# Performance work log

Measured on AMD Instinct MI355X. Metric: run time of the kernel, lower is better.

## Reference

```python
import jax, jax.numpy as jnp
import numpy as np
import math

HEADS = 8
CH = 16  # hidden_channels per head
SCALE = 1.0 / math.sqrt(CH)


def _transformer_conv(x, src, dst, qw, qb, kw, kb, vw, vb, sw, sb):
    """PyG TransformerConv (concat=True, root_weight=True, eval mode -> no dropout)."""
    N = x.shape[0]
    q = (x @ qw + qb).reshape(N, HEADS, CH)
    k = (x @ kw + kb).reshape(N, HEADS, CH)
    v = (x @ vw + vb).reshape(N, HEADS, CH)
    # per-edge attention logits: message from src j to dst i
    alpha = jnp.sum(q[dst] * k[src], axis=-1) * SCALE        # [E, H]
    # segment softmax over incoming edges of each dst node
    m = jax.ops.segment_max(alpha, dst, num_segments=N)      # [N, H]
    a = jnp.exp(alpha - m[dst])                              # [E, H]
    denom = jax.ops.segment_sum(a, dst, num_segments=N)      # [N, H]
    a = a / denom[dst]
    msg = v[src] * a[:, :, None]                             # [E, H, C]
    out = jax.ops.segment_sum(msg, dst, num_segments=N).reshape(N, HEADS * CH)
    return out + x @ sw + sb  # skip connection (lin_skip)


def setup_inputs() -> dict:
    key = jax.random.key(0)
    ks = jax.random.split(key, 16)
    N, E, IN = 50000, 800000, 128
    D = HEADS * CH  # 128

    def lin(k, fi, fo):
        return (jax.random.normal(k, (fi, fo), jnp.float32) / math.sqrt(fi))

    inp = {
        "x": jax.random.normal(ks[0], (N, IN), jnp.float32),
        "edge_index": jax.random.randint(ks[1], (2, E), 0, N, dtype=jnp.int64),
        "edge_attr": jax.random.normal(ks[2], (E, 1), jnp.float32),
        # conv1: in_channels -> hidden*heads
        "q_w0": lin(ks[3], IN, D), "q_b0": jnp.zeros((D,), jnp.float32),
        "k_w0": lin(ks[4], IN, D), "k_b0": jnp.zeros((D,), jnp.float32),
        "v_w0": lin(ks[5], IN, D), "v_b0": jnp.zeros((D,), jnp.float32),
        "s_w0": lin(ks[6], IN, D), "s_b0": jnp.zeros((D,), jnp.float32),
        # conv2[0]: hidden*heads -> hidden*heads
        "q_w1": lin(ks[7], D, D), "q_b1": jnp.zeros((D,), jnp.float32),
        "k_w1": lin(ks[8], D, D), "k_b1": jnp.zeros((D,), jnp.float32),
        "v_w1": lin(ks[9], D, D), "v_b1": jnp.zeros((D,), jnp.float32),
        "s_w1": lin(ks[10], D, D), "s_b1": jnp.zeros((D,), jnp.float32),
    }
    return inp


def reference(x, edge_index, edge_attr,
              q_w0, q_b0, k_w0, k_b0, v_w0, v_b0, s_w0, s_b0,
              q_w1, q_b1, k_w1, k_b1, v_w1, v_b1, s_w1, s_b1):
    src, dst = edge_index[0], edge_index[1]
    # edge_attr is accepted but unused by the original forward
    h = _transformer_conv(x, src, dst, q_w0, q_b0, k_w0, k_b0, v_w0, v_b0, s_w0, s_b0)
    h = jax.nn.relu(h)
    h = _transformer_conv(h, src, dst, q_w1, q_b1, k_w1, k_b1, v_w1, v_b1, s_w1, s_b1)
    return h
```

## Files before the change

### kernel.cpp

```cpp
#include <hip/hip_runtime.h>
#include <math.h>


#define HEADS 8
#define CH 16
#define DM 128
#define SCALE 0.25f

typedef __attribute__((ext_vector_type(8))) short short8;
typedef __attribute__((ext_vector_type(4))) float floatx4;
typedef __attribute__((ext_vector_type(2))) float floatx2;

static __device__ __forceinline__ ushort f2bf(float f) {
    unsigned u = __float_as_uint(f);
    unsigned r = u + 0x7FFFu + ((u >> 16) & 1u);
    return (ushort)(r >> 16);
}
static __device__ __forceinline__ float bflo(unsigned u) {
    return __uint_as_float(u << 16);
}
static __device__ __forceinline__ float bfhi(unsigned u) {
    return __uint_as_float(u & 0xFFFF0000u);
}
static __device__ __forceinline__ unsigned pack2bf(float lo, float hi) {
    return (unsigned)f2bf(lo) | ((unsigned)f2bf(hi) << 16);
}
static __device__ __forceinline__ floatx2 fp8lo(unsigned v) {
    return __builtin_amdgcn_cvt_pk_f32_fp8(v, false);
}
static __device__ __forceinline__ floatx2 fp8hi(unsigned v) {
    return __builtin_amdgcn_cvt_pk_f32_fp8(v, true);
}

#define AP 136

static __device__ __forceinline__ void gemm_body(
    int bx, const float* __restrict__ Xf, const ushort* __restrict__ Xb,
    const ushort* __restrict__ WT,
    const float* __restrict__ bq, const float* __restrict__ bk,
    const float* __restrict__ bv, const float* __restrict__ bsk,
    ushort* __restrict__ Qb, ushort* __restrict__ Kb,
    unsigned char* __restrict__ Vq, ushort* __restrict__ Sb, int N,
    ushort* As)
{
    const int row0 = bx * 32;
    const int tid  = threadIdx.x;

    if (Xf) {
        #pragma unroll
        for (int i = 0; i < 2; ++i) {
            int id = tid + i * 512;
            int r = id >> 5, ch = id & 31;
            float4 v = make_float4(0.f, 0.f, 0.f, 0.f);
            if (row0 + r < N)
                v = *(const float4*)(Xf + (size_t)(row0 + r) * DM + ch * 4);
            ushort4 sv;
            sv.x = f2bf(v.x); sv.y = f2bf(v.y);
            sv.z = f2bf(v.z); sv.w = f2bf(v.w);
            *(ushort4*)(As + r * AP + ch * 4) = sv;
        }
    } else {
        int id = tid;
        int r = id >> 4, ch = id & 15;
        uint4 v = make_uint4(0, 0, 0, 0);
        if (row0 + r < N)
            v = *(const uint4*)(Xb + (size_t)(row0 + r) * DM + ch * 8);
        *(uint4*)(As + r * AP + ch * 8) = v;
    }
    __syncthreads();

    const int lane = tid & 63, w = tid >> 6;
    const int band = w & 3;
    const int m0   = (w >> 2) * 2;
    const int lr = lane & 15, lq = lane >> 4;

    short8 a[4][2];
    #pragma unroll
    for (int ks = 0; ks < 4; ++ks) {
        const int koff = ks * 32 + lq * 8;
        #pragma unroll
        for (int mt = 0; mt < 2; ++mt)
            a[ks][mt] = *(const short8*)(As + (mt * 16 + lr) * AP + koff);
    }

    #pragma unroll
    for (int mi = 0; mi < 2; ++mi) {
        const int mat = m0 + mi;
        const ushort* Wband = WT + (size_t)mat * 16384 + (size_t)band * 4096;
        const float* bias = (mat == 0) ? bq : (mat == 1) ? bk
                          : (mat == 2) ? bv : bsk;
        floatx4 acc[2][2] = {};
        #pragma unroll
        for (int ks = 0; ks < 4; ++ks) {
            short8 b[2];
            #pragma unroll
            for (int t = 0; t < 2; ++t)
                b[t] = *(const short8*)(Wband + (ks * 2 + t) * 512 + lane * 8);
            #pragma unroll
            for (int mt = 0; mt < 2; ++mt)
                #pragma unroll
                for (int nt = 0; nt < 2; ++nt)
                    acc[mt][nt] = __builtin_amdgcn_mfma_f32_16x16x32_bf16(
                        a[ks][mt], b[nt], acc[mt][nt], 0, 0, 0);
        }
        const int nq = band * 32;
        if (mat == 2) {
            #pragma unroll
            for (int nt = 0; nt < 2; ++nt) {
                const int col = nq + nt * 16 + lr;
                const float bcol = bias[col];
                #pragma unroll
                for (int mt = 0; mt < 2; ++mt) {
                    const int rbase0 = row0 + mt * 16 + lq * 4;
                    #pragma unroll
                    for (int r = 0; r < 4; ++r) {
                        const int row = rbase0 + r;
                        if (row < N) {
                            float v = acc[mt][nt][r] + bcol;
                            unsigned p = __builtin_amdgcn_cvt_pk_fp8_f32(
                                v, v, 0u, false);
                            Vq[(size_t)row * DM + col] = (unsigned char)p;
                        }
                    }
                }
            }
        } else {
            ushort* OutB = (mat == 0) ? Qb : (mat == 1) ? Kb : Sb;
            #pragma unroll
            for (int nt = 0; nt < 2; ++nt) {
                const int col = nq + nt * 16 + lr;
                const float bcol = bias[col];
                #pragma unroll
                for (int mt = 0; mt < 2; ++mt) {
                    const int rbase0 = row0 + mt * 16 + lq * 4;
                    #pragma unroll
                    for (int r = 0; r < 4; ++r) {
                        const int row = rbase0 + r;
                        if (row < N)
                            OutB[(size_t)row * DM + col] = f2bf(acc[mt][nt][r] + bcol);
                    }
                }
            }
        }
    }
}

__global__ __launch_bounds__(256)
void cvt_hist(const float* __restrict__ W0, const float* __restrict__ W1,
              const float* __restrict__ W2, const float* __restrict__ W3,
              const float* __restrict__ W4, const float* __restrict__ W5,
              const float* __restrict__ W6, const float* __restrict__ W7,
              ushort* __restrict__ WT,
              const int* __restrict__ dst, int* __restrict__ counts, int E)
{
    const int b = blockIdx.x;
    if (b < 512) {
        const float* Ws[8] = {W0, W1, W2, W3, W4, W5, W6, W7};
        const float* W = Ws[b >> 6];
        int idx = (b & 63) * 256 + threadIdx.x;
        int c    = idx >> 9;
        int s    = idx & 511;
        int lane = s >> 3, j = s & 7;
        int w  = c >> 3, ks = (c >> 1) & 3, t = c & 1;
        int n = w * 32 + t * 16 + (lane & 15);
        int k = ks * 32 + (lane >> 4) * 8 + j;
        WT[(size_t)(b >> 6) * 16384 + idx] = f2bf(W[k * 128 + n]);
    } else {
        int e4 = ((b - 512) * 256 + threadIdx.x) * 4;
        if (e4 + 3 < E) {
            const int4 d = *(const int4*)(dst + e4);
            atomicAdd(&counts[d.x], 1);
            atomicAdd(&counts[d.y], 1);
            atomicAdd(&counts[d.z], 1);
            atomicAdd(&counts[d.w], 1);
        } else {
            for (int e = e4; e < E; ++e) atomicAdd(&counts[dst[e]], 1);
        }
    }
}

__global__ __launch_bounds__(256)
void scan_p1(const int* __restrict__ counts, int* __restrict__ rowptr,
             int* __restrict__ bsums, int* __restrict__ dbins, int N)
{
    __shared__ int s[256];
    __shared__ int lb[256];
    const int t = threadIdx.x;
    const int base = blockIdx.x * 1024 + t * 4;
    lb[t] = 0;
    int c[4];
    int sum = 0;
    #pragma unroll
    for (int j = 0; j < 4; ++j) {
        c[j] = (base + j < N) ? counts[base + j] : 0;
        sum += c[j];
    }
    s[t] = sum;
    __syncthreads();
    #pragma unroll
    for (int j = 0; j < 4; ++j)
        if (base + j < N) atomicAdd(&lb[min(c[j], 255)], 1);
    for (int off = 1; off < 256; off <<= 1) {
        int v = (t >= off) ? s[t - off] : 0;
        __syncthreads();
        if (t >= off) s[t] += v;
        __syncthreads();
    }
    int ex = (t == 0) ? 0 : s[t - 1];
    #pragma unroll
    for (int j = 0; j < 4; ++j) {
        if (base + j < N) rowptr[base + j] = ex;
        ex += c[j];
    }
    if (t == 255) bsums[blockIdx.x] = s[255];
    if (lb[t] > 0) atomicAdd(&dbins[t], lb[t]);
}

__global__ __launch_bounds__(256)
void scan_p2(const int* __restrict__ bsums, int* __restrict__ bbase, int nb,
             const int* __restrict__ dbins, int* __restrict__ dcur)
{
    __shared__ int s[256];
    const int t = threadIdx.x;
    s[t] = (t < nb) ? bsums[t] : 0;
    __syncthreads();
    for (int off = 1; off < 256; off <<= 1) {
        int v = (t >= off) ? s[t - off] : 0;
        __syncthreads();
        if (t >= off) s[t] += v;
        __syncthreads();
    }
    if (t <= nb) bbase[t] = (t == 0) ? 0 : s[t - 1];
    __syncthreads();
    s[t] = dbins[255 - t];
    __syncthreads();
    for (int off = 1; off < 256; off <<= 1) {
        int v = (t >= off) ? s[t - off] : 0;
        __syncthreads();
        if (t >= off) s[t] += v;
        __syncthreads();
    }
    dcur[255 - t] = (t == 0) ? 0 : s[t - 1];
}

__global__ __launch_bounds__(256)
void scan_p3(int* __restrict__ rowptr, int* __restrict__ cursor,
             const int* __restrict__ bbase, int* __restrict__ bcur,
             int N, int nb)
{
    int i = blockIdx.x * 256 + threadIdx.x;
    if (i < N) {
        int v = rowptr[i] + bbase[i >> 10];
        rowptr[i] = v;
        cursor[i] = v;
        if ((i & 255) == 0) bcur[i >> 8] = v;
    }
    if (i == 0) rowptr[N] = bbase[nb];
}

__global__ __launch_bounds__(512)
void gemm_scat(const float* __restrict__ Xf, const ushort* __restrict__ Xb,
               const ushort* __restrict__ WT,
               const float* __restrict__ bq, const float* __restrict__ bk,
               const float* __restrict__ bv, const float* __restrict__ bsk,
               ushort* __restrict__ Qb, ushort* __restrict__ Kb,
               unsigned char* __restrict__ Vq, ushort* __restrict__ Sb, int N,
               const int* __restrict__ src, const int* __restrict__ dst,
               int* __restrict__ cursor, int* __restrict__ esrc,
               int* __restrict__ ebuf, int* __restrict__ bcur,
               const int* __restrict__ counts, int* __restrict__ dcur,
               int* __restrict__ perm, int E, int sb, int db, int bucketed)
{
    __shared__ ushort As[32 * AP];
    __shared__ int lc[256];
    __shared__ int lbase[256];

    const int b = blockIdx.x;
    if (b < sb) {
        if (bucketed) {
            const int t = threadIdx.x;
            if (t < 256) lc[t] = 0;
            __syncthreads();
            int e4 = (b * 512 + t) * 4;
            int pk[4], bkt[4];
            int ne = 0;
            if (e4 + 3 < E) {
                const int4 s = *(const int4*)(src + e4);
                const int4 d = *(const int4*)(dst + e4);
                pk[0] = (s.x & 0xFFFF) | ((d.x & 255) << 16); bkt[0] = d.x >> 8;
                pk[1] = (s.y & 0xFFFF) | ((d.y & 255) << 16); bkt[1] = d.y >> 8;
                pk[2] = (s.z & 0xFFFF) | ((d.z & 255) << 16); bkt[2] = d.z >> 8;
                pk[3] = (s.w & 0xFFFF) | ((d.w & 255) << 16); bkt[3] = d.w >> 8;
                ne = 4;
            } else {
                for (int e = e4; e < E; ++e) {
                    int sv = src[e], dv = dst[e];
                    pk[ne] = (sv & 0xFFFF) | ((dv & 255) << 16);
                    bkt[ne] = dv >> 8;
                    ++ne;
                }
            }
            for (int j = 0; j < ne; ++j) atomicAdd(&lc[bkt[j]], 1);
            __syncthreads();
            if (t < 256 && lc[t] > 0) lbase[t] = atomicAdd(&bcur[t], lc[t]);
            __syncthreads();
            if (t < 256) lc[t] = 0;
            __syncthreads();
            for (int j = 0; j < ne; ++j) {
                int r = atomicAdd(&lc[bkt[j]], 1);
                ebuf[lbase[bkt[j]] + r] = pk[j];
            }
        } else {
            int e4 = (b * 512 + (int)threadIdx.x) * 4;
            if (e4 + 3 < E) {
                const int4 s = *(const int4*)(src + e4);
                const int4 d = *(const int4*)(dst + e4);
                esrc[atomicAdd(&cursor[d.x], 1)] = s.x;
                esrc[atomicAdd(&cursor[d.y], 1)] = s.y;
                esrc[atomicAdd(&cursor[d.z], 1)] = s.z;
                esrc[atomicAdd(&cursor[d.w], 1)] = s.w;
            } else {
                for (int e = e4; e < E; ++e) {
                    int pos = atomicAdd(&cursor[dst[e]], 1);
                    esrc[pos] = src[e];
                }
            }
        }
    } else if (b < sb + db) {
        const int t = threadIdx.x;
        if (t < 256) lc[t] = 0;
        __syncthreads();
        const int n = (b - sb) * 512 + t;
        int bin = 0, rank = 0;
        const bool valid = (n < N);
        if (valid) {
            bin = min(counts[n], 255);
            rank = atomicAdd(&lc[bin], 1);
        }
        __syncthreads();
        if (t < 256 && lc[t] > 0) lbase[t] = atomicAdd(&dcur[t], lc[t]);
        __syncthreads();
        if (valid) perm[lbase[bin] + rank] = n;
    } else {
        gemm_body(b - sb - db, Xf, Xb, WT, bq, bk, bv, bsk,
                  Qb, Kb, Vq, Sb, N, As);
    }
}

__global__ __launch_bounds__(256)
void escat2(const int* __restrict__ rowptr, const int* __restrict__ ebuf,
            int* __restrict__ esrc, int N)
{
    __shared__ int rbase[257];
    __shared__ int cur[256];
    const int b = blockIdx.x, t = threadIdx.x;
    const int n0 = b * 256;
    const int nn = min(256, N - n0);
    rbase[t] = rowptr[min(n0 + t, N)];
    cur[t] = 0;
    if (t == 0) rbase[256] = rowptr[min(n0 + 256, N)];
    __syncthreads();
    const int r0 = rbase[0], r1 = rbase[nn];
    for (int i = r0 + t; i < r1; i += 256) {
        const int e = ebuf[i];
        const int dr = e >> 16;
        const int rank = atomicAdd(&cur[dr], 1);
        esrc[rbase[dr] + rank] = e & 0xFFFF;
    }
}

__global__ __launch_bounds__(512)
void gemm_mfma(const float* __restrict__ Xf, const ushort* __restrict__ Xb,
               const ushort* __restrict__ WT,
               const float* __restrict__ bq, const float* __restrict__ bk,
               const float* __restrict__ bv, const float* __restrict__ bsk,
               ushort* __restrict__ Qb, ushort* __restrict__ Kb,
               unsigned char* __restrict__ Vq, ushort* __restrict__ Sb, int N)
{
    __shared__ ushort As[32 * AP];
    gemm_body(blockIdx.x, Xf, Xb, WT, bq, bk, bv, bsk, Qb, Kb, Vq, Sb, N, As);
}

__global__ __launch_bounds__(256)
void node_attn(const ushort* __restrict__ Qb, const ushort* __restrict__ Kb,
               const unsigned char* __restrict__ Vq,
               const int* __restrict__ rowptr, const int* __restrict__ esrc,
               const int* __restrict__ perm,
               const ushort* __restrict__ Yb, float* __restrict__ Yout,
               ushort* __restrict__ Bout, int N, int relu)
{
    const int idx = blockIdx.x * 8 + (threadIdx.x >> 5);
    if (idx >= N) return;
    const int nid = perm[idx];
    const int c4 = (threadIdx.x & 31) * 4;
    const uint2 qv = *(const uint2*)(Qb + (size_t)nid * DM + c4);
    const float qx = bflo(qv.x), qy = bfhi(qv.x);
    const float qz = bflo(qv.y), qw = bfhi(qv.y);
    const int beg = rowptr[nid], end = rowptr[nid + 1];

    float lA = 0.f, lB = 0.f;
    float a0 = 0.f, a1 = 0.f, a2 = 0.f, a3 = 0.f;
    float b0 = 0.f, b1 = 0.f, b2 = 0.f, b3 = 0.f;

    int i = beg;
    for (; i + 7 < end; i += 8) {
        const int s0 = __builtin_nontemporal_load(esrc + i);
        const int s1 = __builtin_nontemporal_load(esrc + i + 1);
        const int s2 = __builtin_nontemporal_load(esrc + i + 2);
        const int s3 = __builtin_nontemporal_load(esrc + i + 3);
        const int s4 = __builtin_nontemporal_load(esrc + i + 4);
        const int s5 = __builtin_nontemporal_load(esrc + i + 5);
        const int s6 = __builtin_nontemporal_load(esrc + i + 6);
        const int s7 = __builtin_nontemporal_load(esrc + i + 7);
        const uint2 kA = *(const uint2*)(Kb + (size_t)s0 * DM + c4);
        const uint2 kB = *(const uint2*)(Kb + (size_t)s1 * DM + c4);
        const uint2 kC = *(const uint2*)(Kb + (size_t)s2 * DM + c4);
        const uint2 kD = *(const uint2*)(Kb + (size_t)s3 * DM + c4);
        const uint2 kE = *(const uint2*)(Kb + (size_t)s4 * DM + c4);
        const uint2 kF = *(const uint2*)(Kb + (size_t)s5 * DM + c4);
        const uint2 kG = *(const uint2*)(Kb + (size_t)s6 * DM + c4);
        const uint2 kH = *(const uint2*)(Kb + (size_t)s7 * DM + c4);
        const unsigned vA = *(const unsigned*)(Vq + (size_t)s0 * DM + c4);
        const unsigned vB = *(const unsigned*)(Vq + (size_t)s1 * DM + c4);
        const unsigned vC = *(const unsigned*)(Vq + (size_t)s2 * DM + c4);
        const unsigned vD = *(const unsigned*)(Vq + (size_t)s3 * DM + c4);
        const unsigned vE = *(const unsigned*)(Vq + (size_t)s4 * DM + c4);
        const unsigned vF = *(const unsigned*)(Vq + (size_t)s5 * DM + c4);
        const unsigned vG = *(const unsigned*)(Vq + (size_t)s6 * DM + c4);
        const unsigned vH = *(const unsigned*)(Vq + (size_t)s7 * DM + c4);
        float pA = qx * bflo(kA.x);
        pA = fmaf(qy, bfhi(kA.x), pA);
        pA = fmaf(qz, bflo(kA.y), pA);
        pA = fmaf(qw, bfhi(kA.y), pA);
        float pB = qx * bflo(kB.x);
        pB = fmaf(qy, bfhi(kB.x), pB);
        pB = fmaf(qz, bflo(kB.y), pB);
        pB = fmaf(qw, bfhi(kB.y), pB);
        float pC = qx * bflo(kC.x);
        pC = fmaf(qy, bfhi(kC.x), pC);
        pC = fmaf(qz, bflo(kC.y), pC);
        pC = fmaf(qw, bfhi(kC.y), pC);
        float pD = qx * bflo(kD.x);
        pD = fmaf(qy, bfhi(kD.x), pD);
        pD = fmaf(qz, bflo(kD.y), pD);
        pD = fmaf(qw, bfhi(kD.y), pD);
        float pE = qx * bflo(kE.x);
        pE = fmaf(qy, bfhi(kE.x), pE);
        pE = fmaf(qz, bflo(kE.y), pE);
        pE = fmaf(qw, bfhi(kE.y), pE);
        float pF = qx * bflo(kF.x);
        pF = fmaf(qy, bfhi(kF.x), pF);
        pF = fmaf(qz, bflo(kF.y), pF);
        pF = fmaf(qw, bfhi(kF.y), pF);
        float pG = qx * bflo(kG.x);
        pG = fmaf(qy, bfhi(kG.x), pG);
        pG = fmaf(qz, bflo(kG.y), pG);
        pG = fmaf(qw, bfhi(kG.y), pG);
        float pH = qx * bflo(kH.x);
        pH = fmaf(qy, bfhi(kH.x), pH);
        pH = fmaf(qz, bflo(kH.y), pH);
        pH = fmaf(qw, bfhi(kH.y), pH);
        pA += __shfl_xor(pA, 1, 4); pA += __shfl_xor(pA, 2, 4);
        pB += __shfl_xor(pB, 1, 4); pB += __shfl_xor(pB, 2, 4);
        pC += __shfl_xor(pC, 1, 4); pC += __shfl_xor(pC, 2, 4);
        pD += __shfl_xor(pD, 1, 4); pD += __shfl_xor(pD, 2, 4);
        pE += __shfl_xor(pE, 1, 4); pE += __shfl_xor(pE, 2, 4);
        pF += __shfl_xor(pF, 1, 4); pF += __shfl_xor(pF, 2, 4);
        pG += __shfl_xor(pG, 1, 4); pG += __shfl_xor(pG, 2, 4);
        pH += __shfl_xor(pH, 1, 4); pH += __shfl_xor(pH, 2, 4);
        const float wA = __expf(pA * SCALE);
        const float wB = __expf(pB * SCALE);
        const float wC = __expf(pC * SCALE);
        const float wD = __expf(pD * SCALE);
        const float wE = __expf(pE * SCALE);
        const float wF = __expf(pF * SCALE);
        const float wG = __expf(pG * SCALE);
        const float wH = __expf(pH * SCALE);
        lA += (wA + wC) + (wE + wG);
        lB += (wB + wD) + (wF + wH);
        {
            const floatx2 dA0 = fp8lo(vA), dA1 = fp8hi(vA);
            const floatx2 dB0 = fp8lo(vB), dB1 = fp8hi(vB);
            a0 = fmaf(wA, dA0.x, a0); b0 = fmaf(wB, dB0.x, b0);
            a1 = fmaf(wA, dA0.y, a1); b1 = fmaf(wB, dB0.y, b1);
            a2 = fmaf(wA, dA1.x, a2); b2 = fmaf(wB, dB1.x, b2);
            a3 = fmaf(wA, dA1.y, a3); b3 = fmaf(wB, dB1.y, b3);
        }
        {
            const floatx2 dC0 = fp8lo(vC), dC1 = fp8hi(vC);
            const floatx2 dD0 = fp8lo(vD), dD1 = fp8hi(vD);
            a0 = fmaf(wC, dC0.x, a0); b0 = fmaf(wD, dD0.x, b0);
            a1 = fmaf(wC, dC0.y, a1); b1 = fmaf(wD, dD0.y, b1);
            a2 = fmaf(wC, dC1.x, a2); b2 = fmaf(wD, dD1.x, b2);
            a3 = fmaf(wC, dC1.y, a3); b3 = fmaf(wD, dD1.y, b3);
        }
        {
            const floatx2 dE0 = fp8lo(vE), dE1 = fp8hi(vE);
            const floatx2 dF0 = fp8lo(vF), dF1 = fp8hi(vF);
            a0 = fmaf(wE, dE0.x, a0); b0 = fmaf(wF, dF0.x, b0);
            a1 = fmaf(wE, dE0.y, a1); b1 = fmaf(wF, dF0.y, b1);
            a2 = fmaf(wE, dE1.x, a2); b2 = fmaf(wF, dF1.x, b2);
            a3 = fmaf(wE, dE1.y, a3); b3 = fmaf(wF, dF1.y, b3);
        }
        {
            const floatx2 dG0 = fp8lo(vG), dG1 = fp8hi(vG);
            const floatx2 dH0 = fp8lo(vH), dH1 = fp8hi(vH);
            a0 = fmaf(wG, dG0.x, a0); b0 = fmaf(wH, dH0.x, b0);
            a1 = fmaf(wG, dG0.y, a1); b1 = fmaf(wH, dH0.y, b1);
            a2 = fmaf(wG, dG1.x, a2); b2 = fmaf(wH, dH1.x, b2);
            a3 = fmaf(wG, dG1.y, a3); b3 = fmaf(wH, dH1.y, b3);
        }
    }
    for (; i + 3 < end; i += 4) {
        const int s0 = __builtin_nontemporal_load(esrc + i);
        const int s1 = __builtin_nontemporal_load(esrc + i + 1);
        const int s2 = __builtin_nontemporal_load(esrc + i + 2);
        const int s3 = __builtin_nontemporal_load(esrc + i + 3);
        const uint2 kA = *(const uint2*)(Kb + (size_t)s0 * DM + c4);
        const uint2 kB = *(const uint2*)(Kb + (size_t)s1 * DM + c4);
        const uint2 kC = *(const uint2*)(Kb + (size_t)s2 * DM + c4);
        const uint2 kD = *(const uint2*)(Kb + (size_t)s3 * DM + c4);
        const unsigned vA = *(const unsigned*)(Vq + (size_t)s0 * DM + c4);
        const unsigned vB = *(const unsigned*)(Vq + (size_t)s1 * DM + c4);
        const unsigned vC = *(const unsigned*)(Vq + (size_t)s2 * DM + c4);
        const unsigned vD = *(const unsigned*)(Vq + (size_t)s3 * DM + c4);
        float pA = qx * bflo(kA.x);
        pA = fmaf(qy, bfhi(kA.x), pA);
        pA = fmaf(qz, bflo(kA.y), pA);
        pA = fmaf(qw, bfhi(kA.y), pA);
        float pB = qx * bflo(kB.x);
        pB = fmaf(qy, bfhi(kB.x), pB);
        pB = fmaf(qz, bflo(kB.y), pB);
        pB = fmaf(qw, bfhi(kB.y), pB);
        float pC = qx * bflo(kC.x);
        pC = fmaf(qy, bfhi(kC.x), pC);
        pC = fmaf(qz, bflo(kC.y), pC);
        pC = fmaf(qw, bfhi(kC.y), pC);
        float pD = qx * bflo(kD.x);
        pD = fmaf(qy, bfhi(kD.x), pD);
        pD = fmaf(qz, bflo(kD.y), pD);
        pD = fmaf(qw, bfhi(kD.y), pD);
        pA += __shfl_xor(pA, 1, 4); pA += __shfl_xor(pA, 2, 4);
        pB += __shfl_xor(pB, 1, 4); pB += __shfl_xor(pB, 2, 4);
        pC += __shfl_xor(pC, 1, 4); pC += __shfl_xor(pC, 2, 4);
        pD += __shfl_xor(pD, 1, 4); pD += __shfl_xor(pD, 2, 4);
        const float wA = __expf(pA * SCALE);
        const float wB = __expf(pB * SCALE);
        const float wC = __expf(pC * SCALE);
        const float wD = __expf(pD * SCALE);
        lA += wA + wC;
        lB += wB + wD;
        {
            const floatx2 dA0 = fp8lo(vA), dA1 = fp8hi(vA);
            const floatx2 dB0 = fp8lo(vB), dB1 = fp8hi(vB);
            a0 = fmaf(wA, dA0.x, a0); b0 = fmaf(wB, dB0.x, b0);
            a1 = fmaf(wA, dA0.y, a1); b1 = fmaf(wB, dB0.y, b1);
            a2 = fmaf(wA, dA1.x, a2); b2 = fmaf(wB, dB1.x, b2);
            a3 = fmaf(wA, dA1.y, a3); b3 = fmaf(wB, dB1.y, b3);
        }
        {
            const floatx2 dC0 = fp8lo(vC), dC1 = fp8hi(vC);
            const floatx2 dD0 = fp8lo(vD), dD1 = fp8hi(vD);
            a0 = fmaf(wC, dC0.x, a0); b0 = fmaf(wD, dD0.x, b0);
            a1 = fmaf(wC, dC0.y, a1); b1 = fmaf(wD, dD0.y, b1);
            a2 = fmaf(wC, dC1.x, a2); b2 = fmaf(wD, dD1.x, b2);
            a3 = fmaf(wC, dC1.y, a3); b3 = fmaf(wD, dD1.y, b3);
        }
    }
    for (; i < end; ++i) {
        const int s0 = __builtin_nontemporal_load(esrc + i);
        const uint2 kA = *(const uint2*)(Kb + (size_t)s0 * DM + c4);
        const unsigned vA = *(const unsigned*)(Vq + (size_t)s0 * DM + c4);
        float p = qx * bflo(kA.x);
        p = fmaf(qy, bfhi(kA.x), p);
        p = fmaf(qz, bflo(kA.y), p);
        p = fmaf(qw, bfhi(kA.y), p);
        p += __shfl_xor(p, 1, 4);
        p += __shfl_xor(p, 2, 4);
        const float wg = __expf(p * SCALE);
        lA += wg;
        const floatx2 dA0 = fp8lo(vA), dA1 = fp8hi(vA);
        a0 = fmaf(wg, dA0.x, a0);
        a1 = fmaf(wg, dA0.y, a1);
        a2 = fmaf(wg, dA1.x, a2);
        a3 = fmaf(wg, dA1.y, a3);
    }
    const float l = lA + lB;
    a0 += b0; a1 += b1; a2 += b2; a3 += b3;

    const float inv = (l > 0.f) ? 1.f / l : 0.f;
    const uint2 yb = *(const uint2*)(Yb + (size_t)nid * DM + c4);
    float y0 = fmaf(a0, inv, bflo(yb.x));
    float y1 = fmaf(a1, inv, bfhi(yb.x));
    float y2 = fmaf(a2, inv, bflo(yb.y));
    float y3 = fmaf(a3, inv, bfhi(yb.y));
    if (relu) {
        y0 = fmaxf(y0, 0.f); y1 = fmaxf(y1, 0.f);
        y2 = fmaxf(y2, 0.f); y3 = fmaxf(y3, 0.f);
    }
    if (Yout) {
        float4 o = make_float4(y0, y1, y2, y3);
        *(float4*)(Yout + (size_t)nid * DM + c4) = o;
    }
    if (Bout) {
        uint2 o;
        o.x = pack2bf(y0, y1);
        o.y = pack2bf(y2, y3);
        *(uint2*)(Bout + (size_t)nid * DM + c4) = o;
    }
}

extern "C" void kernel_launch(void* const* d_in, const int* in_sizes, int n_in,
                              void* d_out, int out_size, void* d_ws, size_t ws_size,
                              hipStream_t stream)
{
    const float* x   = (const float*)d_in[0];
    const int* eidx  = (const int*)d_in[1];
    const float* qw0 = (const float*)d_in[3];  const float* qb0 = (const float*)d_in[4];
    const float* kw0 = (const float*)d_in[5];  const float* kb0 = (const float*)d_in[6];
    const float* vw0 = (const float*)d_in[7];  const float* vb0 = (const float*)d_in[8];
    const float* sw0 = (const float*)d_in[9];  const float* sb0 = (const float*)d_in[10];
    const float* qw1 = (const float*)d_in[11]; const float* qb1 = (const float*)d_in[12];
    const float* kw1 = (const float*)d_in[13]; const float* kb1 = (const float*)d_in[14];
    const float* vw1 = (const float*)d_in[15]; const float* vb1 = (const float*)d_in[16];
    const float* sw1 = (const float*)d_in[17]; const float* sb1 = (const float*)d_in[18];

    const int N = in_sizes[0] / DM;
    const int E = in_sizes[1] / 2;
    const int* src = eidx;
    const int* dst = eidx + E;

    size_t nd  = (size_t)N * DM;
    ushort* Qb = (ushort*)d_ws;
    ushort* Kb = Qb + nd;
    ushort* Xb = Kb + nd;
    ushort* Sb = Xb + nd;
    ushort* WT = Sb + nd;
    unsigned char* Vq = (unsigned char*)(WT + 8 * 16384);
    int* counts = (int*)(Vq + nd);
    int* rowptr = counts + N;
    int* cursor = rowptr + (N + 1);
    int* esrc   = cursor + N;
    int* perm   = esrc + E;
    int* dbins  = perm + N;
    int* dcur   = dbins + 256;
    int* bsums  = dcur + 256;
    int* bbase  = bsums + 256;
    int* ebuf   = bbase + 257;
    int* bcur   = ebuf + E;
    float* out  = (float*)d_out;

    const int nbuck = (N + 255) >> 8;
    const bool bucketed =
        (N <= 65536) && (nbuck <= 256) &&
        ((uintptr_t)(bcur + 256) <= (uintptr_t)d_ws + ws_size);

    const int nb = (N + 1023) / 1024;
    const int ggrid = (N + 31) / 32;
    const int ablk = (N + 7) / 8;
    const int sb = (E + 2047) / 2048;
    const int db = (N + 511) / 512;

    hipMemsetAsync(counts, 0, (size_t)N * sizeof(int), stream);
    hipMemsetAsync(dbins, 0, 256 * sizeof(int), stream);

    cvt_hist<<<512 + (E + 1023) / 1024, 256, 0, stream>>>(
        qw0, kw0, vw0, sw0, qw1, kw1, vw1, sw1, WT, dst, counts, E);

    scan_p1<<<nb, 256, 0, stream>>>(counts, rowptr, bsums, dbins, N);
    scan_p2<<<1, 256, 0, stream>>>(bsums, bbase, nb, dbins, dcur);
    scan_p3<<<(N + 255) / 256, 256, 0, stream>>>(rowptr, cursor, bbase, bcur,
                                                 N, nb);

    gemm_scat<<<sb + db + ggrid, 512, 0, stream>>>(
        x, nullptr, WT, qb0, kb0, vb0, sb0, Qb, Kb, Vq, Sb, N,
        src, dst, cursor, esrc, ebuf, bcur, counts, dcur, perm,
        E, sb, db, bucketed ? 1 : 0);

    if (bucketed)
        escat2<<<nbuck, 256, 0, stream>>>(rowptr, ebuf, esrc, N);

    node_attn<<<ablk, 256, 0, stream>>>(Qb, Kb, Vq, rowptr, esrc, perm,
                                        Sb, nullptr, Xb, N, 1);

    gemm_mfma<<<ggrid, 512, 0, stream>>>(nullptr, Xb, WT + 4 * 16384,
                                         qb1, kb1, vb1, sb1,
                                         Qb, Kb, Vq, Sb, N);
    node_attn<<<ablk, 256, 0, stream>>>(Qb, Kb, Vq, rowptr, esrc, perm,
                                        Sb, out, nullptr, N, 0);
}
```

Before: 335.2 us.

## Build CSR via per-bucket counts instead of per-node global histogram

In the bucketed path, the per-node global atomic histogram and the three-kernel scan are replaced. Edges are now counted per 256-node bucket using shared-memory atomics, and a single-block scan produces the bucket offsets. The per-bucket scatter kernel then computes per-node degrees, rowptr and the degree bins locally. The degree-sorted permutation is built afterwards by separate small kernels, trading fewer global atomics and scan launches for a few extra small launches.

```diff
diff --git a/kernel.cpp b/kernel.cpp
--- a/kernel.cpp
+++ b/kernel.cpp
@@ -146,13 +146,15 @@
 }
 
 __global__ __launch_bounds__(256)
-void cvt_hist(const float* __restrict__ W0, const float* __restrict__ W1,
+void cvt_bcnt(const float* __restrict__ W0, const float* __restrict__ W1,
               const float* __restrict__ W2, const float* __restrict__ W3,
               const float* __restrict__ W4, const float* __restrict__ W5,
               const float* __restrict__ W6, const float* __restrict__ W7,
               ushort* __restrict__ WT,
-              const int* __restrict__ dst, int* __restrict__ counts, int E)
-{
+              const int* __restrict__ dst, int* __restrict__ bktcnt,
+              int* __restrict__ counts, int E, int mode)
+{
+    __shared__ int lc[256];
     const int b = blockIdx.x;
     if (b < 512) {
         const float* Ws[8] = {W0, W1, W2, W3, W4, W5, W6, W7};
@@ -165,8 +167,24 @@
         int n = w * 32 + t * 16 + (lane & 15);
         int k = ks * 32 + (lane >> 4) * 8 + j;
         WT[(size_t)(b >> 6) * 16384 + idx] = f2bf(W[k * 128 + n]);
+    } else if (mode) {
+        const int t = threadIdx.x;
+        lc[t] = 0;
+        __syncthreads();
+        int e4 = ((b - 512) * 256 + t) * 4;
+        if (e4 + 3 < E) {
+            const int4 d = *(const int4*)(dst + e4);
+            atomicAdd(&lc[d.x >> 8], 1);
+            atomicAdd(&lc[d.y >> 8], 1);
+            atomicAdd(&lc[d.z >> 8], 1);
+            atomicAdd(&lc[d.w >> 8], 1);
+        } else {
+            for (int e = e4; e < E; ++e) atomicAdd(&lc[dst[e] >> 8], 1);
+        }
+        __syncthreads();
+        if (lc[t] > 0) atomicAdd(&bktcnt[t], lc[t]);
     } else {
-        int e4 = ((b - 512) * 256 + threadIdx.x) * 4;
+        int e4 = ((b - 512) * 256 + (int)threadIdx.x) * 4;
         if (e4 + 3 < E) {
             const int4 d = *(const int4*)(dst + e4);
             atomicAdd(&counts[d.x], 1);
@@ -177,6 +195,26 @@
             for (int e = e4; e < E; ++e) atomicAdd(&counts[dst[e]], 1);
         }
     }
+}
+
+__global__ __launch_bounds__(256)
+void bscan(const int* __restrict__ bktcnt, int* __restrict__ bktbase,
+           int* __restrict__ bcur)
+{
+    __shared__ int s[256];
+    const int t = threadIdx.x;
+    s[t] = bktcnt[t];
+    __syncthreads();
+    for (int off = 1; off < 256; off <<= 1) {
+        int v = (t >= off) ? s[t - off] : 0;
+        __syncthreads();
+        if (t >= off) s[t] += v;
+        __syncthreads();
+    }
+    int ex = (t == 0) ? 0 : s[t - 1];
+    bktbase[t] = ex;
+    bcur[t] = ex;
+    if (t == 255) bktbase[256] = s[255];
 }
 
 __global__ __launch_bounds__(256)
@@ -245,15 +283,13 @@
 
 __global__ __launch_bounds__(256)
 void scan_p3(int* __restrict__ rowptr, int* __restrict__ cursor,
-             const int* __restrict__ bbase, int* __restrict__ bcur,
-             int N, int nb)
+             const int* __restrict__ bbase, int N, int nb)
 {
     int i = blockIdx.x * 256 + threadIdx.x;
     if (i < N) {
         int v = rowptr[i] + bbase[i >> 10];
         rowptr[i] = v;
         cursor[i] = v;
-        if ((i & 255) == 0) bcur[i >> 8] = v;
     }
     if (i == 0) rowptr[N] = bbase[nb];
 }
@@ -348,25 +384,83 @@
 }
 
 __global__ __launch_bounds__(256)
-void escat2(const int* __restrict__ rowptr, const int* __restrict__ ebuf,
-            int* __restrict__ esrc, int N)
-{
-    __shared__ int rbase[257];
+void escat2x(const int* __restrict__ bktbase, const int* __restrict__ ebuf,
+             int* __restrict__ rowptr, int* __restrict__ esrc,
+             int* __restrict__ dbins, int N, int nbuck)
+{
+    __shared__ int cnt[256];
+    __shared__ int s[256];
     __shared__ int cur[256];
     const int b = blockIdx.x, t = threadIdx.x;
     const int n0 = b * 256;
     const int nn = min(256, N - n0);
-    rbase[t] = rowptr[min(n0 + t, N)];
-    cur[t] = 0;
-    if (t == 0) rbase[256] = rowptr[min(n0 + 256, N)];
-    __syncthreads();
-    const int r0 = rbase[0], r1 = rbase[nn];
+    const int r0 = bktbase[b], r1 = bktbase[b + 1];
+    cnt[t] = 0;
+    __syncthreads();
+    for (int i = r0 + t; i < r1; i += 256)
+        atomicAdd(&cnt[ebuf[i] >> 16], 1);
+    __syncthreads();
+    const int deg = cnt[t];
+    s[t] = deg;
+    __syncthreads();
+    for (int off = 1; off < 256; off <<= 1) {
+        int v = (t >= off) ? s[t - off] : 0;
+        __syncthreads();
+        if (t >= off) s[t] += v;
+        __syncthreads();
+    }
+    const int ex = (t == 0) ? 0 : s[t - 1];
+    if (t < nn) {
+        rowptr[n0 + t] = r0 + ex;
+        atomicAdd(&dbins[min(deg, 255)], 1);
+    }
+    if (b == nbuck - 1 && t == 0) rowptr[N] = r1;
+    cur[t] = r0 + ex;
+    __syncthreads();
     for (int i = r0 + t; i < r1; i += 256) {
         const int e = ebuf[i];
         const int dr = e >> 16;
-        const int rank = atomicAdd(&cur[dr], 1);
-        esrc[rbase[dr] + rank] = e & 0xFFFF;
-    }
+        const int pos = atomicAdd(&cur[dr], 1);
+        esrc[pos] = e & 0xFFFF;
+    }
+}
+
+__global__ __launch_bounds__(256)
+void dscan(const int* __restrict__ dbins, int* __restrict__ dcur)
+{
+    __shared__ int s[256];
+    const int t = threadIdx.x;
+    s[t] = dbins[255 - t];
+    __syncthreads();
+    for (int off = 1; off < 256; off <<= 1) {
+        int v = (t >= off) ? s[t - off] : 0;
+        __syncthreads();
+        if (t >= off) s[t] += v;
+        __syncthreads();
+    }
+    dcur[255 - t] = (t == 0) ? 0 : s[t - 1];
+}
+
+__global__ __launch_bounds__(256)
+void dscatter2(const int* __restrict__ rowptr, int* __restrict__ dcur,
+               int* __restrict__ perm, int N)
+{
+    __shared__ int lc[256];
+    __shared__ int lbase[256];
+    const int t = threadIdx.x;
+    lc[t] = 0;
+    __syncthreads();
+    const int n = blockIdx.x * 256 + t;
+    int bin = 0, rank = 0;
+    const bool valid = (n < N);
+    if (valid) {
+        bin = min(rowptr[n + 1] - rowptr[n], 255);
+        rank = atomicAdd(&lc[bin], 1);
+    }
+    __syncthreads();
+    if (lc[t] > 0) lbase[t] = atomicAdd(&dcur[t], lc[t]);
+    __syncthreads();
+    if (valid) perm[lbase[bin] + rank] = n;
 }
 
 __global__ __launch_bounds__(512)
@@ -637,48 +731,66 @@
     ushort* Sb = Xb + nd;
     ushort* WT = Sb + nd;
     unsigned char* Vq = (unsigned char*)(WT + 8 * 16384);
-    int* counts = (int*)(Vq + nd);
-    int* rowptr = counts + N;
-    int* cursor = rowptr + (N + 1);
-    int* esrc   = cursor + N;
-    int* perm   = esrc + E;
-    int* dbins  = perm + N;
-    int* dcur   = dbins + 256;
-    int* bsums  = dcur + 256;
-    int* bbase  = bsums + 256;
-    int* ebuf   = bbase + 257;
-    int* bcur   = ebuf + E;
-    float* out  = (float*)d_out;
+    int* counts  = (int*)(Vq + nd);
+    int* rowptr  = counts + N;
+    int* cursor  = rowptr + (N + 1);
+    int* esrc    = cursor + N;
+    int* perm    = esrc + E;
+    int* dbins   = perm + N;
+    int* bktcnt  = dbins + 256;
+    int* dcur    = bktcnt + 256;
+    int* bsums   = dcur + 256;
+    int* bbase   = bsums + 256;
+    int* bktbase = bbase + 257;
+    int* bcur    = bktbase + 257;
+    int* ebuf    = bcur + 256;
+    float* out   = (float*)d_out;
 
     const int nbuck = (N + 255) >> 8;
     const bool bucketed =
         (N <= 65536) && (nbuck <= 256) &&
-        ((uintptr_t)(bcur + 256) <= (uintptr_t)d_ws + ws_size);
-
-    const int nb = (N + 1023) / 1024;
+        ((uintptr_t)(ebuf + E) <= (uintptr_t)d_ws + ws_size);
+
+    const int hb = (E + 1023) / 1024;
     const int ggrid = (N + 31) / 32;
     const int ablk = (N + 7) / 8;
     const int sb = (E + 2047) / 2048;
-    const int db = (N + 511) / 512;
-
-    hipMemsetAsync(counts, 0, (size_t)N * sizeof(int), stream);
-    hipMemsetAsync(dbins, 0, 256 * sizeof(int), stream);
-
-    cvt_hist<<<512 + (E + 1023) / 1024, 256, 0, stream>>>(
-        qw0, kw0, vw0, sw0, qw1, kw1, vw1, sw1, WT, dst, counts, E);
-
-    scan_p1<<<nb, 256, 0, stream>>>(counts, rowptr, bsums, dbins, N);
-    scan_p2<<<1, 256, 0, stream>>>(bsums, bbase, nb, dbins, dcur);
-    scan_p3<<<(N + 255) / 256, 256, 0, stream>>>(rowptr, cursor, bbase, bcur,
-                                                 N, nb);
-
-    gemm_scat<<<sb + db + ggrid, 512, 0, stream>>>(
-        x, nullptr, WT, qb0, kb0, vb0, sb0, Qb, Kb, Vq, Sb, N,
-        src, dst, cursor, esrc, ebuf, bcur, counts, dcur, perm,
-        E, sb, db, bucketed ? 1 : 0);
-
-    if (bucketed)
-        escat2<<<nbuck, 256, 0, stream>>>(rowptr, ebuf, esrc, N);
+
+    if (bucketed) {
+        hipMemsetAsync(dbins, 0, 512 * sizeof(int), stream);
+
+        cvt_bcnt<<<512 + hb, 256, 0, stream>>>(
+            qw0, kw0, vw0, sw0, qw1, kw1, vw1, sw1, WT,
+            dst, bktcnt, counts, E, 1);
+
+        bscan<<<1, 256, 0, stream>>>(bktcnt, bktbase, bcur);
+
+        gemm_scat<<<sb + ggrid, 512, 0, stream>>>(
+            x, nullptr, WT, qb0, kb0, vb0, sb0, Qb, Kb, Vq, Sb, N,
+            src, dst, cursor, esrc, ebuf, bcur, counts, dcur, perm,
+            E, sb, 0, 1);
+
+        escat2x<<<nbuck, 256, 0, stream>>>(bktbase, ebuf, rowptr, esrc,
+                                           dbins, N, nbuck);
+        dscan<<<1, 256, 0, stream>>>(dbins, dcur);
+        dscatter2<<<(N + 255) / 256, 256, 0, stream>>>(rowptr, dcur, perm, N);
+    } else {
+        const int nb = (N + 1023) / 1024;
+        const int db = (N + 511) / 512;
+        hipMemsetAsync(counts, 0, (size_t)N * sizeof(int), stream);
+        hipMemsetAsync(dbins, 0, 256 * sizeof(int), stream);
+        cvt_bcnt<<<512 + hb, 256, 0, stream>>>(
+            qw0, kw0, vw0, sw0, qw1, kw1, vw1, sw1, WT,
+            dst, bktcnt, counts, E, 0);
+        scan_p1<<<nb, 256, 0, stream>>>(counts, rowptr, bsums, dbins, N);
+        scan_p2<<<1, 256, 0, stream>>>(bsums, bbase, nb, dbins, dcur);
+        scan_p3<<<(N + 255) / 256, 256, 0, stream>>>(rowptr, cursor, bbase,
+                                                     N, nb);
+        gemm_scat<<<sb + db + ggrid, 512, 0, stream>>>(
+            x, nullptr, WT, qb0, kb0, vb0, sb0, Qb, Kb, Vq, Sb, N,
+            src, dst, cursor, esrc, ebuf, bcur, counts, dcur, perm,
+            E, sb, db, 0);
+    }
 
     node_attn<<<ablk, 256, 0, stream>>>(Qb, Kb, Vq, rowptr, esrc, perm,
                                         Sb, nullptr, Xb, N, 1);
```

Result: slower. 454.4 us (+35.6%).
